# Kernel tuning notes

Hardware: AMD Instinct MI355X
Metric: run time of the kernel (lower is better)

The kernel has to match this reference:

```python
import jax, jax.numpy as jnp
import numpy as np

IN_FEATURES = 4096
OUT_FEATURES = 4096
RANK = 32
ALPHA = 1.0
SCALE = ALPHA / RANK


def _kaiming_uniform(key, shape):
    # matches torch.nn.init.kaiming_uniform_(a=sqrt(5)) for a 2D weight:
    # gain = sqrt(2/(1+a^2)) = sqrt(1/3); bound = gain*sqrt(3/fan_in) = 1/sqrt(fan_in)
    fan_in = shape[1]  # torch fan_in of an (in_features, rank) tensor is shape[1]
    bound = 1.0 / np.sqrt(fan_in)
    return jax.random.uniform(key, shape, jnp.float32, -bound, bound)


def setup_inputs() -> dict:
    key = jax.random.key(0)
    kx, ka1, ka2, ka3 = jax.random.split(key, 4)
    x = jax.random.normal(kx, (4, 4096, IN_FEATURES), dtype=jnp.float32)
    A_fast = _kaiming_uniform(ka1, (IN_FEATURES, RANK))
    A_med = _kaiming_uniform(ka2, (IN_FEATURES, RANK))
    A_slow = _kaiming_uniform(ka3, (IN_FEATURES, RANK))
    # B matrices are zero-initialized in the module; use small random values so
    # the output is non-trivial for correctness checking.
    kb1, kb2, kb3 = jax.random.split(jax.random.fold_in(key, 7), 3)
    B_fast = 0.02 * jax.random.normal(kb1, (RANK, OUT_FEATURES), dtype=jnp.float32)
    B_med = 0.02 * jax.random.normal(kb2, (RANK, OUT_FEATURES), dtype=jnp.float32)
    B_slow = 0.02 * jax.random.normal(kb3, (RANK, OUT_FEATURES), dtype=jnp.float32)
    return {"x": x, "A_fast": A_fast, "B_fast": B_fast,
            "A_med": A_med, "B_med": B_med,
            "A_slow": A_slow, "B_slow": B_slow}


def reference(x, A_fast, B_fast, A_med, B_med, A_slow, B_slow):
    # Fused form: concat ranks -> two larger GEMMs, then scale.
    A = jnp.concatenate([A_fast, A_med, A_slow], axis=1)   # [in, 3r]
    B = jnp.concatenate([B_fast, B_med, B_slow], axis=0)   # [3r, out]
    h = jnp.einsum('bsi,ir->bsr', x, A)                    # [B, S, 3r]
    out = jnp.einsum('bsr,ro->bso', h, B) * SCALE          # [B, S, out]
    return out
```

## Files before the change

### kernel.cpp

```cpp
#include <hip/hip_runtime.h>
#include <hip/hip_bf16.h>

typedef __attribute__((ext_vector_type(4))) float f32x4;
typedef __attribute__((ext_vector_type(8))) short bf16x8;

__device__ __forceinline__ unsigned short f2bf(float f) {
  unsigned int u = __builtin_bit_cast(unsigned int, f);
  u += 0x7FFFu + ((u >> 16) & 1u);
  return (unsigned short)(u >> 16);
}

__device__ __forceinline__ void async_ld16(const void* g, void* l) {
  __builtin_amdgcn_global_load_lds(
      (__attribute__((address_space(1))) void*)g,
      (__attribute__((address_space(3))) void*)l, 16, 0, 0);
}

__global__ __launch_bounds__(256) void pack_AB(
    const float* __restrict__ Af, const float* __restrict__ Am,
    const float* __restrict__ As, const float* __restrict__ Bf,
    const float* __restrict__ Bm, const float* __restrict__ Bs,
    short* __restrict__ Apack, short* __restrict__ Bpack)
{
  unsigned idx = blockIdx.x * 256u + threadIdx.x;
  if (idx < 393216u) {
    unsigned j = idx & 7u, lane = (idx >> 3) & 63u, rest = idx >> 9;
    unsigned t = rest % 6u, chunk = rest / 6u;
    unsigned k = chunk * 32u + ((lane >> 4) << 3) + j;
    unsigned c = t * 16u + (lane & 15u);
    float v;
    if (c < 32u)      v = Af[k * 32u + c];
    else if (c < 64u) v = Am[k * 32u + (c - 32u)];
    else              v = As[k * 32u + (c - 64u)];
    Apack[idx] = (short)f2bf(v);
  } else {
    unsigned i2 = idx - 393216u;
    unsigned j = i2 & 7u, lane = (i2 >> 3) & 63u, rest = i2 >> 9;
    unsigned nt = rest & 255u, kc = rest >> 8;
    unsigned k = kc * 32u + ((lane >> 4) << 3) + j;
    unsigned n = nt * 16u + (lane & 15u);
    float v;
    if (k < 32u)      v = Bf[k * 4096u + n];
    else if (k < 64u) v = Bm[(k - 32u) * 4096u + n];
    else              v = Bs[(k - 64u) * 4096u + n];
    Bpack[i2] = (short)f2bf(v * 0.03125f);
  }
}

__global__ __launch_bounds__(256, 4) void lora_fused(
    const float* __restrict__ x, const short* __restrict__ Apack,
    const short* __restrict__ Bpack, float* __restrict__ out)
{
  const int rb  = blockIdx.x;
  const int tid = threadIdx.x;
  const int w = tid >> 6, l = tid & 63;
  const int lm = l & 15, lk = l >> 4;
  const size_t rowbase = (size_t)rb * 16;

  __shared__ __align__(16) float smem[8192];

  auto stage = [&](int s, int b) {
    float* base = smem + b * 4096;
    const float* gx = x + rowbase * 4096 + s * 256;
#pragma unroll
    for (int i = 0; i < 4; ++i) {
      int r = w * 4 + i;
      const float* gp = gx + (size_t)r * 4096 + ((l ^ (r & 7)) << 2);
      async_ld16(gp, base + r * 256);
    }
  };

  f32x4 acc[6];
#pragma unroll
  for (int t = 0; t < 6; ++t) acc[t] = (f32x4){0.f, 0.f, 0.f, 0.f};

  stage(0, 0);
  for (int st = 0; st < 16; ++st) {
    __syncthreads();
    if (st < 15) stage(st + 1, (st + 1) & 1);
    const float* buf = smem + (st & 1) * 4096;
    const float* rowp = buf + lm * 256;
    const int sw = lm & 7;
#pragma unroll
    for (int p = 0; p < 2; ++p) {
      int ksub = w * 2 + p;
      int b0 = ksub * 8 + lk * 2;
      f32x4 xa = *(const f32x4*)(rowp + (((b0)     ^ sw) << 2));
      f32x4 xb = *(const f32x4*)(rowp + (((b0 + 1) ^ sw) << 2));
      bf16x8 xf;
      xf[0] = (short)f2bf(xa[0]); xf[1] = (short)f2bf(xa[1]);
      xf[2] = (short)f2bf(xa[2]); xf[3] = (short)f2bf(xa[3]);
      xf[4] = (short)f2bf(xb[0]); xf[5] = (short)f2bf(xb[1]);
      xf[6] = (short)f2bf(xb[2]); xf[7] = (short)f2bf(xb[3]);
      int kchunk = st * 8 + ksub;
#pragma unroll
      for (int t = 0; t < 6; ++t) {
        bf16x8 av = *(const bf16x8*)(Apack + ((size_t)kchunk * 6 + t) * 512 + l * 8);
        acc[t] = __builtin_amdgcn_mfma_f32_16x16x32_bf16(xf, av, acc[t], 0, 0, 0);
      }
    }
  }
  __syncthreads();

  {
    float* hpw = smem + w * 1600;
#pragma unroll
    for (int t = 0; t < 6; ++t)
#pragma unroll
      for (int q = 0; q < 4; ++q)
        hpw[(lk * 4 + q) * 100 + t * 16 + lm] = acc[t][q];
  }
  __syncthreads();

  if (tid < 192) {
    int r = tid / 12, c8 = tid % 12;
    const float* p = smem + r * 100 + c8 * 8;
    f32x4 s0 = *(const f32x4*)(p)     + *(const f32x4*)(p + 1600)
             + *(const f32x4*)(p + 3200) + *(const f32x4*)(p + 4800);
    f32x4 s1 = *(const f32x4*)(p + 4) + *(const f32x4*)(p + 1604)
             + *(const f32x4*)(p + 3204) + *(const f32x4*)(p + 4804);
    bf16x8 o;
    o[0] = (short)f2bf(s0[0]); o[1] = (short)f2bf(s0[1]);
    o[2] = (short)f2bf(s0[2]); o[3] = (short)f2bf(s0[3]);
    o[4] = (short)f2bf(s1[0]); o[5] = (short)f2bf(s1[1]);
    o[6] = (short)f2bf(s1[2]); o[7] = (short)f2bf(s1[3]);
    short* hfr = (short*)(smem + 6400);
    *(bf16x8*)(hfr + ((c8 >> 2) * 64 + (c8 & 3) * 16 + r) * 8) = o;
  }
  __syncthreads();

  {
    const short* hfr = (const short*)(smem + 6400);
    bf16x8 hf[3];
#pragma unroll
    for (int kc = 0; kc < 3; ++kc)
      hf[kc] = *(const bf16x8*)(hfr + (kc * 64 + l) * 8);

    float* orow = out + (rowbase + lm) * 4096;
#pragma unroll 4
    for (int i = 0; i < 64; ++i) {
      int nt = w * 64 + i;
      f32x4 a = {0.f, 0.f, 0.f, 0.f};
#pragma unroll
      for (int kc = 0; kc < 3; ++kc) {
        bf16x8 bv = *(const bf16x8*)(Bpack + ((size_t)(kc * 256 + nt)) * 512 + l * 8);
        a = __builtin_amdgcn_mfma_f32_16x16x32_bf16(bv, hf[kc], a, 0, 0, 0);
      }
      *(f32x4*)(orow + nt * 16 + lk * 4) = a;
    }
  }
}

extern "C" void kernel_launch(void* const* d_in, const int* in_sizes, int n_in,
                              void* d_out, int out_size, void* d_ws, size_t ws_size,
                              hipStream_t stream) {
  const float* x  = (const float*)d_in[0];
  const float* Af = (const float*)d_in[1];
  const float* Bf = (const float*)d_in[2];
  const float* Am = (const float*)d_in[3];
  const float* Bm = (const float*)d_in[4];
  const float* As = (const float*)d_in[5];
  const float* Bs = (const float*)d_in[6];
  float* out = (float*)d_out;

  char* ws = (char*)d_ws;
  short* Apack = (short*)ws;
  short* Bpack = (short*)(ws + 786432);

  hipLaunchKernelGGL(pack_AB, dim3(3072), dim3(256), 0, stream,
                     Af, Am, As, Bf, Bm, Bs, Apack, Bpack);
  hipLaunchKernelGGL(lora_fused, dim3(1024), dim3(256), 0, stream, x, Apack, Bpack, out);
}
```

Measured before the change: 173.3 us.

## Split fused LoRA kernel into two stages and hand-schedule the x-load pipeline

The single fused kernel becomes two kernels. The first computes the bf16 intermediate h and writes it to workspace. The second reads h and runs the rank-96 up-projection over 2048 blocks, each covering 64 rows and one eighth of the output columns, so more blocks run in parallel on the write-heavy output phase. Stage 1 also replaces the __syncthreads double-buffer loop with explicit s_waitcnt vmcnt(4), s_barrier and sched_barrier fencing, so the next x tile's load overlaps with the current tile's MFMAs. The cost is an extra kernel launch and a global round trip for h, which is small next to the 256 MB output.

```diff
diff --git a/kernel.cpp b/kernel.cpp
--- a/kernel.cpp
+++ b/kernel.cpp
@@ -47,9 +47,9 @@
   }
 }
 
-__global__ __launch_bounds__(256, 4) void lora_fused(
+__global__ __launch_bounds__(256, 4) void lora_stage1(
     const float* __restrict__ x, const short* __restrict__ Apack,
-    const short* __restrict__ Bpack, float* __restrict__ out)
+    short* __restrict__ hg)
 {
   const int rb  = blockIdx.x;
   const int tid = threadIdx.x;
@@ -59,27 +59,22 @@
 
   __shared__ __align__(16) float smem[8192];
 
+  f32x4 acc[6];
+#pragma unroll
+  for (int t = 0; t < 6; ++t) acc[t] = (f32x4){0.f, 0.f, 0.f, 0.f};
+
   auto stage = [&](int s, int b) {
     float* base = smem + b * 4096;
     const float* gx = x + rowbase * 4096 + s * 256;
 #pragma unroll
     for (int i = 0; i < 4; ++i) {
       int r = w * 4 + i;
-      const float* gp = gx + (size_t)r * 4096 + ((l ^ (r & 7)) << 2);
-      async_ld16(gp, base + r * 256);
+      async_ld16(gx + (size_t)r * 4096 + ((l ^ (r & 7)) << 2), base + r * 256);
     }
   };
 
-  f32x4 acc[6];
-#pragma unroll
-  for (int t = 0; t < 6; ++t) acc[t] = (f32x4){0.f, 0.f, 0.f, 0.f};
-
-  stage(0, 0);
-  for (int st = 0; st < 16; ++st) {
-    __syncthreads();
-    if (st < 15) stage(st + 1, (st + 1) & 1);
-    const float* buf = smem + (st & 1) * 4096;
-    const float* rowp = buf + lm * 256;
+  auto consume = [&](int st) {
+    const float* rowp = smem + (st & 1) * 4096 + lm * 256;
     const int sw = lm & 7;
 #pragma unroll
     for (int p = 0; p < 2; ++p) {
@@ -99,7 +94,27 @@
         acc[t] = __builtin_amdgcn_mfma_f32_16x16x32_bf16(xf, av, acc[t], 0, 0, 0);
       }
     }
+  };
+
+  stage(0, 0);
+#pragma unroll 1
+  for (int st = 0; st < 15; ++st) {
+    stage(st + 1, (st + 1) & 1);
+    __builtin_amdgcn_sched_barrier(0);
+    asm volatile("s_waitcnt vmcnt(4)" ::: "memory");
+    __builtin_amdgcn_sched_barrier(0);
+    __builtin_amdgcn_s_barrier();
+    __builtin_amdgcn_sched_barrier(0);
+    consume(st);
+    __builtin_amdgcn_sched_barrier(0);
+    __builtin_amdgcn_s_barrier();
+    __builtin_amdgcn_sched_barrier(0);
   }
+  asm volatile("s_waitcnt vmcnt(0)" ::: "memory");
+  __builtin_amdgcn_sched_barrier(0);
+  __builtin_amdgcn_s_barrier();
+  __builtin_amdgcn_sched_barrier(0);
+  consume(15);
   __syncthreads();
 
   {
@@ -115,39 +130,48 @@
   if (tid < 192) {
     int r = tid / 12, c8 = tid % 12;
     const float* p = smem + r * 100 + c8 * 8;
-    f32x4 s0 = *(const f32x4*)(p)     + *(const f32x4*)(p + 1600)
+    f32x4 s0 = *(const f32x4*)(p)        + *(const f32x4*)(p + 1600)
              + *(const f32x4*)(p + 3200) + *(const f32x4*)(p + 4800);
-    f32x4 s1 = *(const f32x4*)(p + 4) + *(const f32x4*)(p + 1604)
+    f32x4 s1 = *(const f32x4*)(p + 4)    + *(const f32x4*)(p + 1604)
              + *(const f32x4*)(p + 3204) + *(const f32x4*)(p + 4804);
     bf16x8 o;
     o[0] = (short)f2bf(s0[0]); o[1] = (short)f2bf(s0[1]);
     o[2] = (short)f2bf(s0[2]); o[3] = (short)f2bf(s0[3]);
     o[4] = (short)f2bf(s1[0]); o[5] = (short)f2bf(s1[1]);
     o[6] = (short)f2bf(s1[2]); o[7] = (short)f2bf(s1[3]);
-    short* hfr = (short*)(smem + 6400);
-    *(bf16x8*)(hfr + ((c8 >> 2) * 64 + (c8 & 3) * 16 + r) * 8) = o;
+    *(bf16x8*)(hg + ((size_t)rb * 192 + (c8 >> 2) * 64 + (c8 & 3) * 16 + r) * 8) = o;
   }
-  __syncthreads();
+}
 
-  {
-    const short* hfr = (const short*)(smem + 6400);
-    bf16x8 hf[3];
+__global__ __launch_bounds__(256, 8) void lora_stage2(
+    const short* __restrict__ hg, const short* __restrict__ Bpack,
+    float* __restrict__ out)
+{
+  const int rb = blockIdx.x >> 3;
+  const int cb = blockIdx.x & 7;
+  const int tid = threadIdx.x;
+  const int w = tid >> 6, l = tid & 63;
+  const int lm = l & 15, lk = l >> 4;
+  const int tile = rb * 4 + w;
+
+  bf16x8 hf[3];
 #pragma unroll
-    for (int kc = 0; kc < 3; ++kc)
-      hf[kc] = *(const bf16x8*)(hfr + (kc * 64 + l) * 8);
+  for (int kc = 0; kc < 3; ++kc)
+    hf[kc] = *(const bf16x8*)(hg + ((size_t)tile * 192 + kc * 64 + l) * 8);
 
-    float* orow = out + (rowbase + lm) * 4096;
-#pragma unroll 4
-    for (int i = 0; i < 64; ++i) {
-      int nt = w * 64 + i;
-      f32x4 a = {0.f, 0.f, 0.f, 0.f};
+  float* orow = out + ((size_t)tile * 16 + lm) * 4096;
+  const short* bp = Bpack + (size_t)l * 8;
+
+#pragma unroll 2
+  for (int i = 0; i < 32; ++i) {
+    int nt = cb * 32 + i;
+    f32x4 a = {0.f, 0.f, 0.f, 0.f};
 #pragma unroll
-      for (int kc = 0; kc < 3; ++kc) {
-        bf16x8 bv = *(const bf16x8*)(Bpack + ((size_t)(kc * 256 + nt)) * 512 + l * 8);
-        a = __builtin_amdgcn_mfma_f32_16x16x32_bf16(bv, hf[kc], a, 0, 0, 0);
-      }
-      *(f32x4*)(orow + nt * 16 + lk * 4) = a;
+    for (int kc = 0; kc < 3; ++kc) {
+      bf16x8 bv = *(const bf16x8*)(bp + (size_t)(kc * 256 + nt) * 512);
+      a = __builtin_amdgcn_mfma_f32_16x16x32_bf16(bv, hf[kc], a, 0, 0, 0);
     }
+    *(f32x4*)(orow + nt * 16 + lk * 4) = a;
   }
 }
 
@@ -166,8 +190,10 @@
   char* ws = (char*)d_ws;
   short* Apack = (short*)ws;
   short* Bpack = (short*)(ws + 786432);
+  short* hg    = (short*)(ws + 2 * 786432);
 
   hipLaunchKernelGGL(pack_AB, dim3(3072), dim3(256), 0, stream,
                      Af, Am, As, Bf, Bm, Bs, Apack, Bpack);
-  hipLaunchKernelGGL(lora_fused, dim3(1024), dim3(256), 0, stream, x, Apack, Bpack, out);
+  hipLaunchKernelGGL(lora_stage1, dim3(1024), dim3(256), 0, stream, x, Apack, hg);
+  hipLaunchKernelGGL(lora_stage2, dim3(2048), dim3(256), 0, stream, hg, Bpack, out);
 }
```

New measurement: 155.6 us. 1.11x faster.
